# Performance work log

Measured on AMD Instinct MI355X. Metric: run time of the kernel, lower is better.

The kernel has to match this reference:

```python
import jax, jax.numpy as jnp
import numpy as np

BETA = 0.25


def setup_inputs() -> dict:
    key = jax.random.key(0)
    k1, k2 = jax.random.split(key)
    z = jax.random.normal(k1, (16, 64, 32, 32), dtype=jnp.float32)
    emb_w = jax.random.normal(k2, (16384, 64), dtype=jnp.float32)
    return {"z": z, "emb_w": emb_w}


def reference(z, emb_w):
    # z: [b, c, h, w] with c == embed_dim; emb_w: [n_embed, embed_dim]
    b, c, h, w = z.shape
    zc = jnp.transpose(z, (0, 2, 3, 1))          # [b, h, w, c]
    zf = zc.reshape(-1, c)                        # [N, c]
    # squared euclidean distances: ||z||^2 - 2 z E^T + ||E||^2  -> [N, n_embed]
    d = (jnp.sum(zf * zf, axis=1, keepdims=True)
         - 2.0 * (zf @ emb_w.T)
         + jnp.sum(emb_w * emb_w, axis=1))
    idx = jnp.argmin(d, axis=1)                   # [N]
    z_q = emb_w[idx].reshape(zc.shape)            # [b, h, w, c]
    # commitment loss (codebook side detached, eval-mode forward)
    loss = BETA * jnp.mean((jax.lax.stop_gradient(z_q) - zc) ** 2)
    # straight-through estimator
    z_q_ste = zc + jax.lax.stop_gradient(z_q - zc)
    z_q_out = jnp.transpose(z_q_ste, (0, 3, 1, 2))  # back to bchw
    return (z_q_out, loss)
```

## Files before the change

### kernel.cpp

```cpp
#include <hip/hip_runtime.h>
#include <math.h>

#define NQ      16384
#define NE      16384
#define DIM     64
#define QB      256
#define CS1     8
#define CPB1    (NE / CS1)
#define CPW1    (CPB1 / 4)
#define NT1     (CPW1 / 32)
#define THREADS 256
#define EPS     0.4f

typedef _Float16 half8  __attribute__((ext_vector_type(8)));
typedef float    f32x4  __attribute__((ext_vector_type(4)));
typedef float    f32x16 __attribute__((ext_vector_type(16)));
typedef unsigned int       uint32;
typedef unsigned short     uint16;
typedef unsigned long long uint64;

typedef union { f32x16 v; f32x4 q[4]; } nvec16;

#define W_NORMS   0
#define W_PM1     16384
#define W_PM2     147456
#define W_PG      278528
#define W_FINALG  344064
#define W_RLIST   360448
#define W_COUNT   376832
#define W_LOSSP   376848
#define W_RKEY    377104
#define W_ZH1     409872
#define W_ZH2     934160
#define W_EH1     1458448
#define W_EH2     1982736

__device__ inline uint32 fmono(float f) {
    uint32 u = __float_as_uint(f);
    return (u & 0x80000000u) ? ~u : (u | 0x80000000u);
}

__global__ __launch_bounds__(THREADS)
void vq_prep(const float* __restrict__ z, const float* __restrict__ emb,
             _Float16* __restrict__ zh1, _Float16* __restrict__ zh2,
             _Float16* __restrict__ eh1, _Float16* __restrict__ eh2,
             float* __restrict__ norms, uint32* __restrict__ count) {
    if (blockIdx.x == 0 && threadIdx.x == 0) *count = 0u;
    if (blockIdx.x < 256) {
        int gid = blockIdx.x * THREADS + threadIdx.x;
        int e = gid >> 2, p = gid & 3;
        const float4* row = reinterpret_cast<const float4*>(emb + (size_t)e * DIM + p * 16);
        float s = 0.f;
#pragma unroll
        for (int i = 0; i < 4; ++i) {
            float4 v = row[i];
            s = fmaf(v.x, v.x, s); s = fmaf(v.y, v.y, s);
            s = fmaf(v.z, v.z, s); s = fmaf(v.w, v.w, s);
            union { _Float16 h[4]; uint2 u; } p1, p2;
            float f[4] = {-2.f * v.x, -2.f * v.y, -2.f * v.z, -2.f * v.w};
#pragma unroll
            for (int j = 0; j < 4; ++j) {
                _Float16 h1 = (_Float16)f[j];
                p1.h[j] = h1;
                p2.h[j] = (_Float16)(f[j] - (float)h1);
            }
            *reinterpret_cast<uint2*>(eh1 + (size_t)e * DIM + p * 16 + i * 4) = p1.u;
            *reinterpret_cast<uint2*>(eh2 + (size_t)e * DIM + p * 16 + i * 4) = p2.u;
        }
        s += __shfl_xor(s, 1, 64);
        s += __shfl_xor(s, 2, 64);
        if (p == 0) norms[e] = s;
    } else {
        int gid = (blockIdx.x - 256) * THREADS + threadIdx.x;
        int n = gid >> 2, p = gid & 3;
        const float* zp = z + (size_t)(n >> 10) * 65536 + (n & 1023) + (size_t)(p * 16) * 1024;
#pragma unroll
        for (int i4 = 0; i4 < 4; ++i4) {
            union { _Float16 h[4]; uint2 u; } p1, p2;
#pragma unroll
            for (int j = 0; j < 4; ++j) {
                float x = zp[(size_t)(i4 * 4 + j) * 1024];
                _Float16 h1 = (_Float16)x;
                p1.h[j] = h1;
                p2.h[j] = (_Float16)(x - (float)h1);
            }
            *reinterpret_cast<uint2*>(zh1 + (size_t)n * DIM + p * 16 + i4 * 4) = p1.u;
            *reinterpret_cast<uint2*>(zh2 + (size_t)n * DIM + p * 16 + i4 * 4) = p2.u;
        }
    }
}

#define LOADT(AS, TL) {                                                            \
    const _Float16* _pa = eh1 + (size_t)(cwbase + (TL) * 32 + q31) * DIM + hi8;    \
    AS[0] = *reinterpret_cast<const half8*>(_pa);                                  \
    AS[1] = *reinterpret_cast<const half8*>(_pa + 16);                             \
    AS[2] = *reinterpret_cast<const half8*>(_pa + 32);                             \
    AS[3] = *reinterpret_cast<const half8*>(_pa + 48); }

#define LOADSN(SN, TL) {                                                           \
    _Pragma("unroll")                                                              \
    for (int k = 0; k < 32; ++k) SN[k] = nrm_s[(TL) * 32 + k]; }

#define MKNS(NS, SN) {                                                             \
    _Pragma("unroll")                                                              \
    for (int j = 0; j < 16; ++j)                                                   \
        NS.v[j] = hi ? SN[(j >> 2) * 8 + 4 + (j & 3)] : SN[(j >> 2) * 8 + (j & 3)]; }

#define CHAIN(ACC, AS, NS, QG)                                                     \
    __builtin_amdgcn_s_setprio(1);                                                 \
    ACC = __builtin_amdgcn_mfma_f32_32x32x16_f16(AS[0], B[QG][0], NS.v, 0, 0, 0);  \
    ACC = __builtin_amdgcn_mfma_f32_32x32x16_f16(AS[1], B[QG][1], ACC,  0, 0, 0);  \
    ACC = __builtin_amdgcn_mfma_f32_32x32x16_f16(AS[2], B[QG][2], ACC,  0, 0, 0);  \
    ACC = __builtin_amdgcn_mfma_f32_32x32x16_f16(AS[3], B[QG][3], ACC,  0, 0, 0);  \
    __builtin_amdgcn_s_setprio(0);

#define MINTRK(ACC, QG, TID) {                                                     \
    float u0 = fminf(fminf(ACC[0],  ACC[1]),  ACC[2]);                             \
    float u1 = fminf(fminf(ACC[3],  ACC[4]),  ACC[5]);                             \
    float u2 = fminf(fminf(ACC[6],  ACC[7]),  ACC[8]);                             \
    float u3 = fminf(fminf(ACC[9],  ACC[10]), ACC[11]);                            \
    float u4 = fminf(fminf(ACC[12], ACC[13]), ACC[14]);                            \
    float v  = fminf(fminf(fminf(u0, u1), u2), fminf(fminf(u3, u4), ACC[15]));     \
    float nm2 = fminf(m2[QG], fmaxf(v, mv[QG]));                  \
    bool lt = v < mv[QG];                                 \
    mv[QG] = lt ? v : mv[QG];                                                      \
    mi[QG] = lt ? (TID) : mi[QG];                                                  \
    m2[QG] = nm2; }

#define COMPUTE(AS, NS, TL) {                                                      \
    const uint32 _tid = (uint32)(TL);                                              \
    f32x16 aA, aB;                                                                 \
    CHAIN(aA, AS, NS, 0)                                                           \
    CHAIN(aB, AS, NS, 1) MINTRK(aA, 0, _tid)                                       \
    CHAIN(aA, AS, NS, 2) MINTRK(aB, 1, _tid)                                       \
    CHAIN(aB, AS, NS, 3) MINTRK(aA, 2, _tid)                                       \
    CHAIN(aA, AS, NS, 4) MINTRK(aB, 3, _tid)                                       \
    CHAIN(aB, AS, NS, 5) MINTRK(aA, 4, _tid)                                       \
    CHAIN(aA, AS, NS, 6) MINTRK(aB, 5, _tid)                                       \
    CHAIN(aB, AS, NS, 7) MINTRK(aA, 6, _tid)                                       \
    MINTRK(aB, 7, _tid) }

__global__ __launch_bounds__(THREADS, 2)
void vq_pass1(const _Float16* __restrict__ zh1, const _Float16* __restrict__ eh1,
              const float* __restrict__ norms,
              float* __restrict__ pm1, float* __restrict__ pm2, uint16* __restrict__ pg) {
    __shared__ float  redv[4][QB];
    __shared__ float  red2[4][QB];
    __shared__ uint32 redg[4][QB];

    const int t    = threadIdx.x;
    const int lane = t & 63;
    const int wave = t >> 6;
    const int q31  = lane & 31;
    const int hi   = lane >> 5;
    const int hi8  = hi * 8;
    const int qbase  = blockIdx.x * QB;
    const int cwbase = blockIdx.y * CPB1 + wave * CPW1;

    const float* nrm_s = norms + (size_t)__builtin_amdgcn_readfirstlane(cwbase);

    half8 B[8][4];
#pragma unroll
    for (int qg = 0; qg < 8; ++qg)
#pragma unroll
        for (int kc = 0; kc < 4; ++kc)
            B[qg][kc] = *reinterpret_cast<const half8*>(
                zh1 + (size_t)(qbase + qg * 32 + q31) * DIM + kc * 16 + hi8);

    float  mv[8], m2[8];
    uint32 mi[8];
#pragma unroll
    for (int q = 0; q < 8; ++q) { mv[q] = INFINITY; m2[q] = INFINITY; mi[q] = 0u; }

    half8 A0[4], A1[4];
    float sn0[32], sn1[32];

    LOADT(A0, 0) LOADSN(sn0, 0)
    for (int tb = 0; tb < NT1; tb += 2) {
        LOADT(A1, tb + 1) LOADSN(sn1, tb + 1)
        {
            nvec16 N0; MKNS(N0, sn0)
            COMPUTE(A0, N0, tb)
        }
        int nx = (tb + 2 < NT1) ? tb + 2 : 0;
        LOADT(A0, nx) LOADSN(sn0, nx)
        {
            nvec16 N1; MKNS(N1, sn1)
            COMPUTE(A1, N1, tb + 1)
        }
    }

    uint32 gi[8];
#pragma unroll
    for (int qg = 0; qg < 8; ++qg)
        gi[qg] = ((uint32)(cwbase >> 5) + mi[qg]) * 2u + (uint32)hi;

#pragma unroll
    for (int qg = 0; qg < 8; ++qg) {
        float  ov = __shfl_xor(mv[qg], 32, 64);
        float  o2 = __shfl_xor(m2[qg], 32, 64);
        uint32 og = (uint32)__shfl_xor((int)gi[qg], 32, 64);
        float nm2 = fminf(fminf(m2[qg], o2), fmaxf(mv[qg], ov));
        if (ov < mv[qg] || (ov == mv[qg] && og < gi[qg])) { mv[qg] = ov; gi[qg] = og; }
        m2[qg] = nm2;
    }
    if (lane < 32) {
#pragma unroll
        for (int qg = 0; qg < 8; ++qg) {
            redv[wave][qg * 32 + lane] = mv[qg];
            red2[wave][qg * 32 + lane] = m2[qg];
            redg[wave][qg * 32 + lane] = gi[qg];
        }
    }
    __syncthreads();

    {
        float  bv = redv[0][t], b2 = red2[0][t];
        uint32 bg = redg[0][t];
#pragma unroll
        for (int w = 1; w < 4; ++w) {
            float v = redv[w][t], s2 = red2[w][t];
            float nm2 = fminf(fminf(b2, s2), fmaxf(bv, v));
            if (v < bv) { bv = v; bg = redg[w][t]; }
            b2 = nm2;
        }
        pm1[(size_t)blockIdx.y * NQ + qbase + t] = bv;
        pm2[(size_t)blockIdx.y * NQ + qbase + t] = b2;
        pg [(size_t)blockIdx.y * NQ + qbase + t] = (uint16)bg;
    }
}

__global__ __launch_bounds__(THREADS)
void vq_select(const float* __restrict__ pm1, const float* __restrict__ pm2,
               const uint16* __restrict__ pg,
               uint32* __restrict__ final_g, uint32* __restrict__ rlist,
               uint32* __restrict__ count, uint64* __restrict__ rkey) {
    const int n = blockIdx.x * THREADS + threadIdx.x;
    float M1 = INFINITY, M2 = INFINITY;
    uint32 G = 0u;
#pragma unroll
    for (int s = 0; s < CS1; ++s) {
        float  m1  = pm1[(size_t)s * NQ + n];
        float  m2s = pm2[(size_t)s * NQ + n];
        uint32 g   = (uint32)pg[(size_t)s * NQ + n];
        float nm2 = fminf(fminf(M2, m2s), fmaxf(M1, m1));
        if (m1 < M1) { M1 = m1; G = g; }
        M2 = nm2;
    }
    rkey[n] = ~0ull;
    if (M2 - M1 > EPS) {
        final_g[n] = G;
    } else {
        final_g[n] = 0xFFFFFFFFu;
        uint32 p = atomicAdd(count, 1u);
        rlist[p] = (uint32)n;
    }
}

__global__ __launch_bounds__(THREADS, 2)
void vq_rescue(const _Float16* __restrict__ zh1, const _Float16* __restrict__ zh2,
               const _Float16* __restrict__ eh1, const _Float16* __restrict__ eh2,
               const float* __restrict__ norms,
               const uint32* __restrict__ rlist, const uint32* __restrict__ countp,
               uint64* __restrict__ rkey) {
    __shared__ float  redv[4][128];
    __shared__ uint32 redg[4][128];

    const uint32 count = *countp;
    const uint32 nch   = (count + 127u) >> 7;
    const int t    = threadIdx.x;
    const int lane = t & 63;
    const int wave = t >> 6;
    const int r15  = lane & 15, hk = lane >> 4;
    const int cy   = blockIdx.x & 15;
    const int rcb  = cy * 1024 + wave * 256;

    for (uint32 cx = (uint32)(blockIdx.x >> 4); cx < nch; cx += 32u) {
        half8 B1[8][2], B2[8][2];
#pragma unroll
        for (int qt = 0; qt < 8; ++qt) {
            uint32 j = cx * 128u + (uint32)(qt * 16 + r15);
            uint32 qid = (j < count) ? rlist[j] : 0u;
#pragma unroll
            for (int kc = 0; kc < 2; ++kc) {
                size_t off = (size_t)qid * DIM + kc * 32 + hk * 8;
                B1[qt][kc] = *reinterpret_cast<const half8*>(zh1 + off);
                B2[qt][kc] = *reinterpret_cast<const half8*>(zh2 + off);
            }
        }

        float  mv[8];
        uint32 mi[8];
#pragma unroll
        for (int q = 0; q < 8; ++q) { mv[q] = INFINITY; mi[q] = 0u; }

        half8 a1[2], a2[2];
        f32x4 nc;
        {
            const _Float16* p1 = eh1 + (size_t)(rcb + r15) * DIM + hk * 8;
            const _Float16* p2 = eh2 + (size_t)(rcb + r15) * DIM + hk * 8;
            a1[0] = *reinterpret_cast<const half8*>(p1);
            a1[1] = *reinterpret_cast<const half8*>(p1 + 32);
            a2[0] = *reinterpret_cast<const half8*>(p2);
            a2[1] = *reinterpret_cast<const half8*>(p2 + 32);
            nc = *reinterpret_cast<const f32x4*>(norms + rcb + hk * 4);
        }

#pragma unroll 2
        for (int tile = 0; tile < 16; ++tile) {
            int nt = (tile + 1 < 16) ? tile + 1 : tile;
            half8 b1[2], b2[2];
            f32x4 nn;
            {
                const _Float16* p1 = eh1 + (size_t)(rcb + nt * 16 + r15) * DIM + hk * 8;
                const _Float16* p2 = eh2 + (size_t)(rcb + nt * 16 + r15) * DIM + hk * 8;
                b1[0] = *reinterpret_cast<const half8*>(p1);
                b1[1] = *reinterpret_cast<const half8*>(p1 + 32);
                b2[0] = *reinterpret_cast<const half8*>(p2);
                b2[1] = *reinterpret_cast<const half8*>(p2 + 32);
                nn = *reinterpret_cast<const f32x4*>(norms + rcb + nt * 16 + hk * 4);
            }

            f32x4 acc[8];
            __builtin_amdgcn_s_setprio(1);
#pragma unroll
            for (int qt = 0; qt < 8; ++qt) {
                acc[qt] = __builtin_amdgcn_mfma_f32_16x16x32_f16(a1[0], B1[qt][0], nc,      0, 0, 0);
                acc[qt] = __builtin_amdgcn_mfma_f32_16x16x32_f16(a1[1], B1[qt][1], acc[qt], 0, 0, 0);
                acc[qt] = __builtin_amdgcn_mfma_f32_16x16x32_f16(a1[0], B2[qt][0], acc[qt], 0, 0, 0);
                acc[qt] = __builtin_amdgcn_mfma_f32_16x16x32_f16(a1[1], B2[qt][1], acc[qt], 0, 0, 0);
                acc[qt] = __builtin_amdgcn_mfma_f32_16x16x32_f16(a2[0], B1[qt][0], acc[qt], 0, 0, 0);
                acc[qt] = __builtin_amdgcn_mfma_f32_16x16x32_f16(a2[1], B1[qt][1], acc[qt], 0, 0, 0);
            }
            __builtin_amdgcn_s_setprio(0);

            const uint32 tid = (uint32)tile;
#pragma unroll
            for (int qt = 0; qt < 8; ++qt) {
                float v = fminf(fminf(fminf(acc[qt][0], acc[qt][1]), acc[qt][2]), acc[qt][3]);
                bool lt = v < mv[qt];
                mv[qt] = lt ? v : mv[qt];
                mi[qt] = lt ? tid : mi[qt];
            }
            a1[0] = b1[0]; a1[1] = b1[1];
            a2[0] = b2[0]; a2[1] = b2[1];
            nc = nn;
        }

        uint32 gi[8];
#pragma unroll
        for (int q = 0; q < 8; ++q)
            gi[q] = (uint32)(rcb >> 2) + (mi[q] << 2) + (uint32)hk;
#pragma unroll
        for (int st = 16; st < 64; st <<= 1) {
#pragma unroll
            for (int q = 0; q < 8; ++q) {
                float  ov = __shfl_xor(mv[q], st, 64);
                uint32 og = (uint32)__shfl_xor((int)gi[q], st, 64);
                if (ov < mv[q] || (ov == mv[q] && og < gi[q])) { mv[q] = ov; gi[q] = og; }
            }
        }
        if (lane < 16) {
#pragma unroll
            for (int qt = 0; qt < 8; ++qt) {
                redv[wave][qt * 16 + lane] = mv[qt];
                redg[wave][qt * 16 + lane] = gi[qt];
            }
        }
        __syncthreads();
        if (t < 128) {
            float  bv = redv[0][t];
            uint32 bg = redg[0][t];
#pragma unroll
            for (int w = 1; w < 4; ++w) {
                float v = redv[w][t];
                if (v < bv) { bv = v; bg = redg[w][t]; }
            }
            uint32 j = cx * 128u + (uint32)t;
            if (j < count) {
                uint64 key = ((uint64)fmono(bv) << 32) | (uint64)bg;
                atomicMin(rkey + rlist[j], key);
            }
        }
        __syncthreads();
    }
}

__global__ __launch_bounds__(THREADS)
void vq_finalize(const float* __restrict__ z,
                 const float* __restrict__ emb,
                 const float* __restrict__ norms,
                 const uint32* __restrict__ final_g,
                 const uint64* __restrict__ rkey,
                 float* __restrict__ out,
                 float* __restrict__ lossp) {
    const int t  = threadIdx.x;
    const int ql = t >> 2, p = t & 3;
    const int n  = blockIdx.x * 64 + ql;
    const int c0 = p * 16;

    uint32 bg = final_g[n];
    if (bg == 0xFFFFFFFFu) {
        uint32 c4 = (uint32)(rkey[n] & 0xFFFFFFFFull) * 4u;
        bg = (c4 >> 5) * 2u + ((c4 >> 2) & 1u);
    }
    const int gbase = (int)((bg >> 1) * 32u + (bg & 1u) * 4u);

    const float* zp = z + (size_t)(n >> 10) * 65536 + (n & 1023);
    float zq[16];
#pragma unroll
    for (int c = 0; c < 16; ++c) zq[c] = zp[(size_t)(c0 + c) * 1024];

    float dp[16];
#pragma unroll
    for (int j = 0; j < 16; ++j) {
        int code = gbase + (j & 3) + 8 * (j >> 2);
        const float4* er = reinterpret_cast<const float4*>(emb + (size_t)code * DIM + c0);
        float d = 0.f;
#pragma unroll
        for (int i = 0; i < 4; ++i) {
            float4 e4 = er[i];
            d = fmaf(e4.x, zq[i * 4 + 0], d);
            d = fmaf(e4.y, zq[i * 4 + 1], d);
            d = fmaf(e4.z, zq[i * 4 + 2], d);
            d = fmaf(e4.w, zq[i * 4 + 3], d);
        }
        dp[j] = d;
    }
#pragma unroll
    for (int st = 1; st < 4; st <<= 1) {
#pragma unroll
        for (int j = 0; j < 16; ++j) dp[j] += __shfl_xor(dp[j], st, 64);
    }

    f32x4 nr[4];
#pragma unroll
    for (int k = 0; k < 4; ++k)
        nr[k] = *reinterpret_cast<const f32x4*>(norms + gbase + k * 8);

    float bs = INFINITY;
    uint32 bi = 0u;
#pragma unroll
    for (int j = 0; j < 16; ++j) {
        float s = fmaf(-2.f, dp[j], nr[j >> 2][j & 3]);
        uint32 code = (uint32)(gbase + (j & 3) + 8 * (j >> 2));
        if (s < bs) { bs = s; bi = code; }
    }

    const float* ew = emb + (size_t)bi * DIM + c0;
    float* op = out + (size_t)(n >> 10) * 65536 + (n & 1023);

    float ls = 0.f;
#pragma unroll
    for (int c = 0; c < 16; ++c) {
        float e = ew[c];
        op[(size_t)(c0 + c) * 1024] = e;
        float d = e - zq[c];
        ls = fmaf(d, d, ls);
    }

#pragma unroll
    for (int off = 32; off > 0; off >>= 1) ls += __shfl_down(ls, off, 64);
    __shared__ float wsum[THREADS / 64];
    if ((t & 63) == 0) wsum[t >> 6] = ls;
    __syncthreads();
    if (t == 0) {
        float s = 0.f;
#pragma unroll
        for (int w = 0; w < THREADS / 64; ++w) s += wsum[w];
        lossp[blockIdx.x] = s;
    }
}

__global__ __launch_bounds__(64)
void vq_loss_final(const float* __restrict__ lossp, float* __restrict__ out) {
    float v = 0.f;
#pragma unroll
    for (int k = 0; k < 4; ++k) v += lossp[threadIdx.x + k * 64];
#pragma unroll
    for (int off = 32; off > 0; off >>= 1) v += __shfl_down(v, off, 64);
    if (threadIdx.x == 0)
        out[1048576] = 0.25f * v / 1048576.0f;
}

extern "C" void kernel_launch(void* const* d_in, const int* in_sizes, int n_in,
                              void* d_out, int out_size, void* d_ws, size_t ws_size,
                              hipStream_t stream) {
    const float* z   = (const float*)d_in[0];
    const float* emb = (const float*)d_in[1];
    float* out = (float*)d_out;

    float* ws = (float*)d_ws;
    float*     norms   = ws + W_NORMS;
    float*     pm1     = ws + W_PM1;
    float*     pm2     = ws + W_PM2;
    uint16*    pg      = (uint16*)(ws + W_PG);
    uint32*    final_g = (uint32*)(ws + W_FINALG);
    uint32*    rlist   = (uint32*)(ws + W_RLIST);
    uint32*    count   = (uint32*)(ws + W_COUNT);
    float*     lossp   = ws + W_LOSSP;
    uint64*    rkey    = (uint64*)(ws + W_RKEY);
    _Float16*  zh1     = (_Float16*)(ws + W_ZH1);
    _Float16*  zh2     = (_Float16*)(ws + W_ZH2);
    _Float16*  eh1     = (_Float16*)(ws + W_EH1);
    _Float16*  eh2     = (_Float16*)(ws + W_EH2);

    vq_prep<<<512, THREADS, 0, stream>>>(z, emb, zh1, zh2, eh1, eh2, norms, count);

    dim3 g1(NQ / QB, CS1);
    vq_pass1<<<g1, THREADS, 0, stream>>>(zh1, eh1, norms, pm1, pm2, pg);

    vq_select<<<NQ / THREADS, THREADS, 0, stream>>>(pm1, pm2, pg, final_g, rlist, count, rkey);

    vq_rescue<<<512, THREADS, 0, stream>>>(zh1, zh2, eh1, eh2, norms, rlist, count, rkey);

    vq_finalize<<<NQ / 64, THREADS, 0, stream>>>(z, emb, norms, final_g, rkey, out, lossp);
    vq_loss_final<<<1, 64, 0, stream>>>(lossp, out);
}
```

Measured before the change: 98.35 us.

## Single-buffer pass1 tile loop and fold loss reduction into finalize via last-block atomic

The pass1 main loop moves from double-buffered A0/A1 register tiles to a single buffer. The next tile's loads are issued after the last MFMA chain, overlapping only with the final min-tracking step. This cuts register pressure, which may help occupancy, but hides less load latency. Separately, the vq_loss_final kernel is removed: the last finalize block, found with an atomic counter that prep resets, sums the per-block loss partials, saving one kernel launch.

```diff
diff --git a/kernel.cpp b/kernel.cpp
--- a/kernel.cpp
+++ b/kernel.cpp
@@ -45,7 +45,7 @@
              _Float16* __restrict__ zh1, _Float16* __restrict__ zh2,
              _Float16* __restrict__ eh1, _Float16* __restrict__ eh2,
              float* __restrict__ norms, uint32* __restrict__ count) {
-    if (blockIdx.x == 0 && threadIdx.x == 0) *count = 0u;
+    if (blockIdx.x == 0 && threadIdx.x == 0) { count[0] = 0u; count[1] = 0u; }
     if (blockIdx.x < 256) {
         int gid = blockIdx.x * THREADS + threadIdx.x;
         int e = gid >> 2, p = gid & 3;
@@ -127,19 +127,6 @@
     mi[QG] = lt ? (TID) : mi[QG];                                                  \
     m2[QG] = nm2; }
 
-#define COMPUTE(AS, NS, TL) {                                                      \
-    const uint32 _tid = (uint32)(TL);                                              \
-    f32x16 aA, aB;                                                                 \
-    CHAIN(aA, AS, NS, 0)                                                           \
-    CHAIN(aB, AS, NS, 1) MINTRK(aA, 0, _tid)                                       \
-    CHAIN(aA, AS, NS, 2) MINTRK(aB, 1, _tid)                                       \
-    CHAIN(aB, AS, NS, 3) MINTRK(aA, 2, _tid)                                       \
-    CHAIN(aA, AS, NS, 4) MINTRK(aB, 3, _tid)                                       \
-    CHAIN(aB, AS, NS, 5) MINTRK(aA, 4, _tid)                                       \
-    CHAIN(aA, AS, NS, 6) MINTRK(aB, 5, _tid)                                       \
-    CHAIN(aB, AS, NS, 7) MINTRK(aA, 6, _tid)                                       \
-    MINTRK(aB, 7, _tid) }
-
 __global__ __launch_bounds__(THREADS, 2)
 void vq_pass1(const _Float16* __restrict__ zh1, const _Float16* __restrict__ eh1,
               const float* __restrict__ norms,
@@ -172,22 +159,25 @@
 #pragma unroll
     for (int q = 0; q < 8; ++q) { mv[q] = INFINITY; m2[q] = INFINITY; mi[q] = 0u; }
 
-    half8 A0[4], A1[4];
-    float sn0[32], sn1[32];
-
-    LOADT(A0, 0) LOADSN(sn0, 0)
-    for (int tb = 0; tb < NT1; tb += 2) {
-        LOADT(A1, tb + 1) LOADSN(sn1, tb + 1)
-        {
-            nvec16 N0; MKNS(N0, sn0)
-            COMPUTE(A0, N0, tb)
-        }
-        int nx = (tb + 2 < NT1) ? tb + 2 : 0;
-        LOADT(A0, nx) LOADSN(sn0, nx)
-        {
-            nvec16 N1; MKNS(N1, sn1)
-            COMPUTE(A1, N1, tb + 1)
-        }
+    half8 A[4];
+    float sn[32];
+
+    LOADT(A, 0) LOADSN(sn, 0)
+    for (int tl = 0; tl < NT1; ++tl) {
+        const uint32 _tid = (uint32)tl;
+        nvec16 N; MKNS(N, sn)
+        f32x16 aA, aB;
+        CHAIN(aA, A, N, 0)
+        CHAIN(aB, A, N, 1) MINTRK(aA, 0, _tid)
+        CHAIN(aA, A, N, 2) MINTRK(aB, 1, _tid)
+        CHAIN(aB, A, N, 3) MINTRK(aA, 2, _tid)
+        CHAIN(aA, A, N, 4) MINTRK(aB, 3, _tid)
+        CHAIN(aB, A, N, 5) MINTRK(aA, 4, _tid)
+        CHAIN(aA, A, N, 6) MINTRK(aB, 5, _tid)
+        CHAIN(aB, A, N, 7) MINTRK(aA, 6, _tid)
+        int nx = (tl + 1 < NT1) ? tl + 1 : 0;
+        LOADT(A, nx) LOADSN(sn, nx)
+        MINTRK(aB, 7, _tid)
     }
 
     uint32 gi[8];
@@ -393,7 +383,8 @@
                  const uint32* __restrict__ final_g,
                  const uint64* __restrict__ rkey,
                  float* __restrict__ out,
-                 float* __restrict__ lossp) {
+                 float* __restrict__ lossp,
+                 uint32* __restrict__ done) {
     const int t  = threadIdx.x;
     const int ql = t >> 2, p = t & 3;
     const int n  = blockIdx.x * 64 + ql;
@@ -469,18 +460,16 @@
 #pragma unroll
         for (int w = 0; w < THREADS / 64; ++w) s += wsum[w];
         lossp[blockIdx.x] = s;
-    }
-}
-
-__global__ __launch_bounds__(64)
-void vq_loss_final(const float* __restrict__ lossp, float* __restrict__ out) {
-    float v = 0.f;
-#pragma unroll
-    for (int k = 0; k < 4; ++k) v += lossp[threadIdx.x + k * 64];
-#pragma unroll
-    for (int off = 32; off > 0; off >>= 1) v += __shfl_down(v, off, 64);
-    if (threadIdx.x == 0)
-        out[1048576] = 0.25f * v / 1048576.0f;
+        __threadfence();
+        uint32 old = atomicAdd(done, 1u);
+        if (old == 255u) {
+            float tot = 0.f;
+            for (int i = 0; i < 256; ++i)
+                tot += __hip_atomic_load(lossp + i, __ATOMIC_RELAXED,
+                                         __HIP_MEMORY_SCOPE_AGENT);
+            out[1048576] = 0.25f * tot / 1048576.0f;
+        }
+    }
 }
 
 extern "C" void kernel_launch(void* const* d_in, const int* in_sizes, int n_in,
@@ -514,6 +503,6 @@
 
     vq_rescue<<<512, THREADS, 0, stream>>>(zh1, zh2, eh1, eh2, norms, rlist, count, rkey);
 
-    vq_finalize<<<NQ / 64, THREADS, 0, stream>>>(z, emb, norms, final_g, rkey, out, lossp);
-    vq_loss_final<<<1, 64, 0, stream>>>(lossp, out);
-}
+    vq_finalize<<<NQ / 64, THREADS, 0, stream>>>(z, emb, norms, final_g, rkey, out,
+                                                 lossp, count + 1);
+}
```

Measured after the change: 90.74 us. 7.7% less time.
